# Optimization experiments

Hardware: AMD Instinct MI355X
Metric: run time of the kernel (lower is better)

Reference implementation:

```python
import jax, jax.numpy as jnp
import numpy as np

N = 4096
C = 8192
D = 64
MARGIN = 0.1
ALPHA = 32.0


def setup_inputs() -> dict:
    key = jax.random.key(0)
    k1, k2, k3, k4 = jax.random.split(key, 4)
    embeddings = jax.random.normal(k1, (N, D), dtype=jnp.float32)
    labels = jax.random.randint(k2, (N,), 0, C)
    # kaiming_normal_(mode='fan_out') on a (C, D) tensor -> std = sqrt(2/C)
    mean_proxies = jax.random.normal(k3, (C, D), dtype=jnp.float32) * np.sqrt(2.0 / C)
    log_variance_proxies = jax.random.normal(k4, (C, D), dtype=jnp.float32) * np.sqrt(2.0 / C)
    return {
        "embeddings": embeddings,
        "labels": labels,
        "mean_proxies": mean_proxies,
        "log_variance_proxies": log_variance_proxies,
    }


def _mls_scores(e, mu, logvar):
    """score[i,j] = -0.5 * sum_d[(e_id - mu_jd)^2 * exp(-logvar_jd) + logvar_jd].
    Expanded into GEMMs to avoid materializing the (N, C, D) broadcast tensor."""
    inv_var = jnp.exp(-logvar)                                  # (C, D)
    e2_term = (e * e) @ inv_var.T                               # (N, C)
    cross = e @ (mu * inv_var).T                                # (N, C)
    const = jnp.sum(mu * mu * inv_var + logvar, axis=1)         # (C,)
    return -0.5 * (e2_term - 2.0 * cross + const[None, :])      # (N, C)


def reference(embeddings, labels, mean_proxies, log_variance_proxies):
    score_mat = _mls_scores(embeddings, mean_proxies, log_variance_proxies)  # (N, C)
    pos_mask = jax.nn.one_hot(labels, C, dtype=score_mat.dtype)              # (N, C)

    pos_e = -ALPHA * (score_mat - MARGIN)
    neg_e = ALPHA * (score_mat + MARGIN)
    m = jnp.max(pos_e)  # NOTE: original code uses max(pos_exp) for BOTH terms
    pos_exp = jnp.exp(pos_e - m)
    neg_exp = jnp.exp(neg_e - m)

    counts = jnp.sum(pos_mask, axis=0)                   # (C,)
    num_valid = jnp.sum(counts != 0).astype(score_mat.dtype)

    pos_sim_sum = jnp.sum(jnp.where(pos_mask == 1, pos_exp, 0.0), axis=0)  # (C,)
    neg_sim_sum = jnp.sum(jnp.where(pos_mask == 0, neg_exp, 0.0), axis=0)  # (C,)

    pos_term = jnp.sum(jnp.log1p(pos_sim_sum) + m) / num_valid
    neg_term = jnp.sum(jnp.log1p(neg_sim_sum) + m) / C
    return pos_term + neg_term
```

## Files before the change

kernel.cpp:

```cpp
#include <hip/hip_runtime.h>
#include <hip/hip_bf16.h>
#include <math.h>


#define N_EMB 4096
#define C_CLS 8192
#define D_DIM 64
#define K_DIM 128

typedef __attribute__((ext_vector_type(8))) __bf16 bf16x8;
typedef __attribute__((ext_vector_type(4))) __bf16 bf16x4;
typedef __attribute__((ext_vector_type(16))) float f32x16;
typedef __attribute__((ext_vector_type(4))) int i32x4;

__device__ __forceinline__ void async_ld16(void* lds, const void* g) {
  __builtin_amdgcn_global_load_lds(
      (__attribute__((address_space(1))) void*)g,
      (__attribute__((address_space(3))) void*)lds, 16, 0, 0);
}

__global__ void k_prep(const float* __restrict__ emb,
                       const float* __restrict__ mp,
                       const float* __restrict__ lvp,
                       __bf16* __restrict__ wsA,
                       __bf16* __restrict__ wsB,
                       float* __restrict__ constv) {
  const int wave = (int)((blockIdx.x * blockDim.x + threadIdx.x) >> 6);
  const int lane = threadIdx.x & 63;
  const int sub = lane >> 4, q = lane & 15;
  const int row = wave * 4 + sub;
  if (row < N_EMB) {
    float4 e4 = *(const float4*)&emb[row * D_DIM + q * 4];
    bf16x4 sq = {(__bf16)(e4.x * e4.x), (__bf16)(e4.y * e4.y),
                 (__bf16)(e4.z * e4.z), (__bf16)(e4.w * e4.w)};
    bf16x4 ev = {(__bf16)e4.x, (__bf16)e4.y, (__bf16)e4.z, (__bf16)e4.w};
    *(bf16x4*)&wsA[row * K_DIM + q * 4] = sq;
    *(bf16x4*)&wsA[row * K_DIM + D_DIM + q * 4] = ev;
  } else {
    const int j = row - N_EMB;
    float4 mu4 = *(const float4*)&mp[j * D_DIM + q * 4];
    float4 lv4 = *(const float4*)&lvp[j * D_DIM + q * 4];
    float iv0 = __expf(-lv4.x), iv1 = __expf(-lv4.y);
    float iv2 = __expf(-lv4.z), iv3 = __expf(-lv4.w);
    bf16x4 ivv = {(__bf16)iv0, (__bf16)iv1, (__bf16)iv2, (__bf16)iv3};
    bf16x4 mv = {(__bf16)(-2.0f * mu4.x * iv0), (__bf16)(-2.0f * mu4.y * iv1),
                 (__bf16)(-2.0f * mu4.z * iv2), (__bf16)(-2.0f * mu4.w * iv3)};
    *(bf16x4*)&wsB[j * K_DIM + q * 4] = ivv;
    *(bf16x4*)&wsB[j * K_DIM + D_DIM + q * 4] = mv;
    float t = fmaf(mu4.x * mu4.x, iv0, lv4.x)
            + fmaf(mu4.y * mu4.y, iv1, lv4.y)
            + fmaf(mu4.z * mu4.z, iv2, lv4.z)
            + fmaf(mu4.w * mu4.w, iv3, lv4.w);
    #pragma unroll
    for (int s = 8; s >= 1; s >>= 1) t += __shfl_xor(t, s);
    if (q == 0) constv[j] = t;
  }
}

__global__ __launch_bounds__(256, 2) void k_main(
    const __bf16* __restrict__ wsA, const __bf16* __restrict__ wsB,
    const float* __restrict__ constv, const int* __restrict__ labels,
    float* __restrict__ wsM, float* __restrict__ wsP, float* __restrict__ wsN) {
  __shared__ __align__(16) char As[32768];
  __shared__ __align__(16) char Bs[32768];

  const int tid = threadIdx.x;
  const int rb = blockIdx.x & 31;
  const int cb = blockIdx.x >> 5;

  const char* Ag = (const char*)(wsA + (size_t)rb * 128 * K_DIM);
  const char* Bg = (const char*)(wsB + (size_t)cb * 128 * K_DIM);
  #pragma unroll
  for (int it = 0; it < 8; ++it) {
    int L = it * 256 + tid;
    int r = L >> 4, cs = L & 15;
    int goff = r * 256 + ((cs ^ (r & 15)) << 4);
    async_ld16(As + L * 16, Ag + goff);
  }
  #pragma unroll
  for (int it = 0; it < 8; ++it) {
    int L = it * 256 + tid;
    int r = L >> 4, cs = L & 15;
    int goff = r * 256 + ((cs ^ (r & 15)) << 4);
    async_ld16(Bs + L * 16, Bg + goff);
  }
  __syncthreads();

  const int wv = tid >> 6, lane = tid & 63;
  const int wr = wv >> 1, wc = wv & 1;
  const int l31 = lane & 31, kg = lane >> 5;
  const int l15 = lane & 15;

  f32x16 acc[2][2];
  #pragma unroll
  for (int mi = 0; mi < 2; ++mi)
    #pragma unroll
    for (int ni = 0; ni < 2; ++ni)
      #pragma unroll
      for (int r = 0; r < 16; ++r) acc[mi][ni][r] = 0.f;

  #pragma unroll
  for (int kk = 0; kk < 8; ++kk) {
    const int c = kk * 2 + kg;
    const int cofs = (c ^ l15) << 4;
    bf16x8 af[2], bfr[2];
    #pragma unroll
    for (int mi = 0; mi < 2; ++mi)
      af[mi] = *(const bf16x8*)(As + (wr * 64 + mi * 32 + l31) * 256 + cofs);
    #pragma unroll
    for (int ni = 0; ni < 2; ++ni)
      bfr[ni] = *(const bf16x8*)(Bs + (wc * 64 + ni * 32 + l31) * 256 + cofs);
    #pragma unroll
    for (int mi = 0; mi < 2; ++mi)
      #pragma unroll
      for (int ni = 0; ni < 2; ++ni)
        acc[mi][ni] = __builtin_amdgcn_mfma_f32_32x32x16_bf16(
            af[mi], bfr[ni], acc[mi][ni], 0, 0, 0);
  }

  __syncthreads();
  float* colred = (float*)As;
  int* labels_s = (int*)(As + 3072);
  float* pc_s   = (float*)(As + 3584);
  if (tid < 128) {
    labels_s[tid] = labels[rb * 128 + tid];
    pc_s[tid] = fmaf(16.0f, constv[cb * 128 + tid], 3.2f);
  }
  __syncthreads();

  i32x4 labv[2][4];
  #pragma unroll
  for (int mi = 0; mi < 2; ++mi)
    #pragma unroll
    for (int g = 0; g < 4; ++g)
      labv[mi][g] = *(const i32x4*)&labels_s[wr * 64 + mi * 32 + 4 * kg + 8 * g];

  #pragma unroll
  for (int ni = 0; ni < 2; ++ni) {
    const int col_local = wc * 64 + ni * 32 + l31;
    const int gcol = cb * 128 + col_local;
    const float pcv = pc_s[col_local];
    float lmax = -1e30f;
    #pragma unroll
    for (int mi = 0; mi < 2; ++mi)
      #pragma unroll
      for (int r = 0; r < 16; ++r)
        lmax = fmaxf(lmax, fmaf(16.0f, acc[mi][ni][r], pcv));
    lmax = fmaxf(lmax, __shfl_xor(lmax, 32));
    float ps = 0.f, ns = 0.f;
    #pragma unroll
    for (int mi = 0; mi < 2; ++mi)
      #pragma unroll
      for (int r = 0; r < 16; ++r) {
        float pe = fmaf(16.0f, acc[mi][ni][r], pcv);
        bool match = (labv[mi][r >> 2][r & 3] == gcol);
        float v = match ? pe : (6.4f - pe);
        float ex = __expf(v - lmax);
        ps += match ? ex : 0.f;
        ns += match ? 0.f : ex;
      }
    ps += __shfl_xor(ps, 32);
    ns += __shfl_xor(ns, 32);
    if (kg == 0) {
      float* cr = &colred[(wr * 128 + col_local) * 3];
      cr[0] = lmax; cr[1] = ps; cr[2] = ns;
    }
  }
  __syncthreads();
  if (tid < 128) {
    const float* c0 = &colred[(0 * 128 + tid) * 3];
    const float* c1 = &colred[(1 * 128 + tid) * 3];
    float M = fmaxf(c0[0], c1[0]);
    float s0 = __expf(c0[0] - M), s1 = __expf(c1[0] - M);
    int gcol = cb * 128 + tid;
    wsM[rb * C_CLS + gcol] = M;
    wsP[rb * C_CLS + gcol] = fmaf(c0[1], s0, c1[1] * s1);
    wsN[rb * C_CLS + gcol] = fmaf(c0[2], s0, c1[2] * s1);
  }
}

__global__ __launch_bounds__(256) void k_red1(
    const float* __restrict__ wsM, const float* __restrict__ wsP,
    const float* __restrict__ wsN, float* __restrict__ Mcol,
    float* __restrict__ Pcol, float* __restrict__ Ncol) {
  __shared__ float red[8][32][3];
  const int tid = threadIdx.x;
  const int col = tid & 31, part = tid >> 5;
  const int j = blockIdx.x * 32 + col;

  float m4[4];
  float M = -1e30f;
  #pragma unroll
  for (int r = 0; r < 4; ++r) {
    m4[r] = wsM[(part * 4 + r) * C_CLS + j];
    M = fmaxf(M, m4[r]);
  }
  float ps = 0.f, ns = 0.f;
  #pragma unroll
  for (int r = 0; r < 4; ++r) {
    float s = __expf(m4[r] - M);
    ps = fmaf(wsP[(part * 4 + r) * C_CLS + j], s, ps);
    ns = fmaf(wsN[(part * 4 + r) * C_CLS + j], s, ns);
  }
  red[part][col][0] = M; red[part][col][1] = ps; red[part][col][2] = ns;
  __syncthreads();
  if (part == 0) {
    float Mx = -1e30f;
    #pragma unroll
    for (int p = 0; p < 8; ++p) Mx = fmaxf(Mx, red[p][col][0]);
    float P = 0.f, Nn = 0.f;
    #pragma unroll
    for (int p = 0; p < 8; ++p) {
      float s = __expf(red[p][col][0] - Mx);
      P = fmaf(red[p][col][1], s, P);
      Nn = fmaf(red[p][col][2], s, Nn);
    }
    Mcol[j] = Mx; Pcol[j] = P; Ncol[j] = Nn;
  }
}

__global__ __launch_bounds__(1024) void k_fin(
    const float* __restrict__ Mcol, const float* __restrict__ Pcol,
    const float* __restrict__ Ncol, const int* __restrict__ labels,
    float* __restrict__ out) {
  __shared__ unsigned char flag[C_CLS];
  __shared__ float sA[16], sB[16];
  __shared__ int sI[16];
  const int tid = threadIdx.x;
  const int wv = tid >> 6, lane = tid & 63;

  float colMv[8], colPv[8], colNv[8];
  #pragma unroll
  for (int k = 0; k < 8; ++k) {
    int i = k * 1024 + tid;
    colMv[k] = Mcol[i]; colPv[k] = Pcol[i]; colNv[k] = Ncol[i];
  }

  for (int i = tid; i < C_CLS; i += 1024) flag[i] = 0;
  __syncthreads();
  for (int i = tid; i < N_EMB; i += 1024) flag[labels[i]] = 1;
  __syncthreads();
  int nv = 0;
  float gm = -1e30f;
  #pragma unroll
  for (int k = 0; k < 8; ++k) {
    nv += flag[k * 1024 + tid];
    gm = fmaxf(gm, colMv[k]);
  }
  #pragma unroll
  for (int s = 32; s >= 1; s >>= 1) {
    gm = fmaxf(gm, __shfl_xor(gm, s));
    nv += __shfl_xor(nv, s);
  }
  if (lane == 0) { sA[wv] = gm; sI[wv] = nv; }
  __syncthreads();
  if (tid == 0) {
    float mm = -1e30f; int n = 0;
    #pragma unroll
    for (int k = 0; k < 16; ++k) { mm = fmaxf(mm, sA[k]); n += sI[k]; }
    sA[0] = mm; sI[0] = n;
  }
  __syncthreads();
  const float m = sA[0];
  const int num_valid = sI[0];
  __syncthreads();
  float pt = 0.f, nt = 0.f;
  #pragma unroll
  for (int k = 0; k < 8; ++k) {
    float s = __expf(colMv[k] - m);
    pt += log1pf(colPv[k] * s);
    nt += log1pf(colNv[k] * s);
  }
  #pragma unroll
  for (int s = 32; s >= 1; s >>= 1) {
    pt += __shfl_xor(pt, s);
    nt += __shfl_xor(nt, s);
  }
  if (lane == 0) { sA[wv] = pt; sB[wv] = nt; }
  __syncthreads();
  if (tid == 0) {
    float sp = 0.f, sn = 0.f;
    #pragma unroll
    for (int k = 0; k < 16; ++k) { sp += sA[k]; sn += sB[k]; }
    out[0] = (sp + (float)C_CLS * m) / (float)num_valid
           + (sn + (float)C_CLS * m) / (float)C_CLS;
  }
}

extern "C" void kernel_launch(void* const* d_in, const int* in_sizes, int n_in,
                              void* d_out, int out_size, void* d_ws, size_t ws_size,
                              hipStream_t stream) {
  const float* emb    = (const float*)d_in[0];
  const int*   labels = (const int*)d_in[1];
  const float* mp     = (const float*)d_in[2];
  const float* lvp    = (const float*)d_in[3];
  float* out = (float*)d_out;

  char* ws = (char*)d_ws;
  __bf16* wsA   = (__bf16*)ws;
  __bf16* wsB   = (__bf16*)(ws + (1u << 20));
  float* constv = (float*)(ws + 3u * (1u << 20));
  float* wsM    = (float*)(ws + 3u * (1u << 20) + (1u << 15));
  float* wsP    = wsM + 32 * C_CLS;
  float* wsN    = wsP + 32 * C_CLS;
  float* Mcol   = wsN + 32 * C_CLS;
  float* Pcol   = Mcol + C_CLS;
  float* Ncol   = Pcol + C_CLS;

  hipLaunchKernelGGL(k_prep, dim3(768), dim3(256), 0, stream,
                     emb, mp, lvp, wsA, wsB, constv);
  hipLaunchKernelGGL(k_main, dim3((N_EMB / 128) * (C_CLS / 128)), dim3(256), 0, stream,
                     wsA, wsB, constv, labels, wsM, wsP, wsN);
  hipLaunchKernelGGL(k_red1, dim3(256), dim3(256), 0, stream,
                     wsM, wsP, wsN, Mcol, Pcol, Ncol);
  hipLaunchKernelGGL(k_fin, dim3(1), dim3(1024), 0, stream,
                     Mcol, Pcol, Ncol, labels, out);
}
```

Baseline: 101.7 us.

## Use base-2 exponent domain, prefetch labels early, distribute valid-class counting to reduction

Rescales the score computation into log2 units so the epilogue uses exp2f directly, storing the scaled scores back into the accumulators and folding the margin into a precomputed bias. Label and constant loads are issued before the barrier to overlap with the async tile loads. The valid-class flag computation moves from the single-block final kernel into the 256-block reduction kernel, which emits per-block counts, removing an 8K shared flag array and serial scatter from k_fin. This adds redundant label scans in each reduction block and changes the rounding behaviour slightly.

```diff
diff --git a/kernel.cpp b/kernel.cpp
--- a/kernel.cpp
+++ b/kernel.cpp
@@ -7,6 +7,11 @@
 #define C_CLS 8192
 #define D_DIM 64
 #define K_DIM 128
+
+#define S2_F    23.083120654223414f
+#define B2_F     4.616624130844683f
+#define NEGC2_F  9.233248261689366f
+#define LN2_F    0.6931471805599453f
 
 typedef __attribute__((ext_vector_type(8))) __bf16 bf16x8;
 typedef __attribute__((ext_vector_type(4))) __bf16 bf16x4;
@@ -84,6 +89,11 @@
     int goff = r * 256 + ((cs ^ (r & 15)) << 4);
     async_ld16(Bs + L * 16, Bg + goff);
   }
+  int lab_r = 0; float cv_r = 0.f;
+  if (tid < 128) {
+    lab_r = labels[rb * 128 + tid];
+    cv_r  = constv[cb * 128 + tid];
+  }
   __syncthreads();
 
   const int wv = tid >> 6, lane = tid & 63;
@@ -123,8 +133,8 @@
   int* labels_s = (int*)(As + 3072);
   float* pc_s   = (float*)(As + 3584);
   if (tid < 128) {
-    labels_s[tid] = labels[rb * 128 + tid];
-    pc_s[tid] = fmaf(16.0f, constv[cb * 128 + tid], 3.2f);
+    labels_s[tid] = lab_r;
+    pc_s[tid] = fmaf(S2_F, cv_r, B2_F);
   }
   __syncthreads();
 
@@ -144,18 +154,22 @@
     #pragma unroll
     for (int mi = 0; mi < 2; ++mi)
       #pragma unroll
-      for (int r = 0; r < 16; ++r)
-        lmax = fmaxf(lmax, fmaf(16.0f, acc[mi][ni][r], pcv));
+      for (int r = 0; r < 16; ++r) {
+        float pe = fmaf(S2_F, acc[mi][ni][r], pcv);
+        acc[mi][ni][r] = pe;
+        lmax = fmaxf(lmax, pe);
+      }
     lmax = fmaxf(lmax, __shfl_xor(lmax, 32));
+    const float negb = NEGC2_F - lmax;
     float ps = 0.f, ns = 0.f;
     #pragma unroll
     for (int mi = 0; mi < 2; ++mi)
       #pragma unroll
       for (int r = 0; r < 16; ++r) {
-        float pe = fmaf(16.0f, acc[mi][ni][r], pcv);
+        float pe = acc[mi][ni][r];
         bool match = (labv[mi][r >> 2][r & 3] == gcol);
-        float v = match ? pe : (6.4f - pe);
-        float ex = __expf(v - lmax);
+        float a = match ? (pe - lmax) : (negb - pe);
+        float ex = exp2f(a);
         ps += match ? ex : 0.f;
         ns += match ? 0.f : ex;
       }
@@ -171,7 +185,7 @@
     const float* c0 = &colred[(0 * 128 + tid) * 3];
     const float* c1 = &colred[(1 * 128 + tid) * 3];
     float M = fmaxf(c0[0], c1[0]);
-    float s0 = __expf(c0[0] - M), s1 = __expf(c1[0] - M);
+    float s0 = exp2f(c0[0] - M), s1 = exp2f(c1[0] - M);
     int gcol = cb * 128 + tid;
     wsM[rb * C_CLS + gcol] = M;
     wsP[rb * C_CLS + gcol] = fmaf(c0[1], s0, c1[1] * s1);
@@ -181,12 +195,17 @@
 
 __global__ __launch_bounds__(256) void k_red1(
     const float* __restrict__ wsM, const float* __restrict__ wsP,
-    const float* __restrict__ wsN, float* __restrict__ Mcol,
-    float* __restrict__ Pcol, float* __restrict__ Ncol) {
+    const float* __restrict__ wsN, const int* __restrict__ labels,
+    float* __restrict__ Mcol, float* __restrict__ Pcol,
+    float* __restrict__ Ncol, int* __restrict__ nvp) {
   __shared__ float red[8][32][3];
+  __shared__ int fl[32];
   const int tid = threadIdx.x;
   const int col = tid & 31, part = tid >> 5;
-  const int j = blockIdx.x * 32 + col;
+  const int bx = blockIdx.x;
+  const int j = bx * 32 + col;
+
+  if (tid < 32) fl[tid] = 0;
 
   float m4[4];
   float M = -1e30f;
@@ -198,12 +217,22 @@
   float ps = 0.f, ns = 0.f;
   #pragma unroll
   for (int r = 0; r < 4; ++r) {
-    float s = __expf(m4[r] - M);
+    float s = exp2f(m4[r] - M);
     ps = fmaf(wsP[(part * 4 + r) * C_CLS + j], s, ps);
     ns = fmaf(wsN[(part * 4 + r) * C_CLS + j], s, ns);
   }
   red[part][col][0] = M; red[part][col][1] = ps; red[part][col][2] = ns;
   __syncthreads();
+
+  #pragma unroll
+  for (int it = 0; it < 4; ++it) {
+    int4 lb = ((const int4*)labels)[it * 256 + tid];
+    if ((lb.x >> 5) == bx) fl[lb.x & 31] = 1;
+    if ((lb.y >> 5) == bx) fl[lb.y & 31] = 1;
+    if ((lb.z >> 5) == bx) fl[lb.z & 31] = 1;
+    if ((lb.w >> 5) == bx) fl[lb.w & 31] = 1;
+  }
+
   if (part == 0) {
     float Mx = -1e30f;
     #pragma unroll
@@ -211,19 +240,25 @@
     float P = 0.f, Nn = 0.f;
     #pragma unroll
     for (int p = 0; p < 8; ++p) {
-      float s = __expf(red[p][col][0] - Mx);
+      float s = exp2f(red[p][col][0] - Mx);
       P = fmaf(red[p][col][1], s, P);
       Nn = fmaf(red[p][col][2], s, Nn);
     }
     Mcol[j] = Mx; Pcol[j] = P; Ncol[j] = Nn;
   }
+  __syncthreads();
+  if (tid < 64) {
+    int f = (tid < 32) ? fl[tid] : 0;
+    #pragma unroll
+    for (int s = 32; s >= 1; s >>= 1) f += __shfl_xor(f, s);
+    if (tid == 0) nvp[bx] = f;
+  }
 }
 
 __global__ __launch_bounds__(1024) void k_fin(
     const float* __restrict__ Mcol, const float* __restrict__ Pcol,
-    const float* __restrict__ Ncol, const int* __restrict__ labels,
+    const float* __restrict__ Ncol, const int* __restrict__ nvp,
     float* __restrict__ out) {
-  __shared__ unsigned char flag[C_CLS];
   __shared__ float sA[16], sB[16];
   __shared__ int sI[16];
   const int tid = threadIdx.x;
@@ -235,18 +270,11 @@
     int i = k * 1024 + tid;
     colMv[k] = Mcol[i]; colPv[k] = Pcol[i]; colNv[k] = Ncol[i];
   }
-
-  for (int i = tid; i < C_CLS; i += 1024) flag[i] = 0;
-  __syncthreads();
-  for (int i = tid; i < N_EMB; i += 1024) flag[labels[i]] = 1;
-  __syncthreads();
-  int nv = 0;
+  int nv = (tid < 256) ? nvp[tid] : 0;
+
   float gm = -1e30f;
   #pragma unroll
-  for (int k = 0; k < 8; ++k) {
-    nv += flag[k * 1024 + tid];
-    gm = fmaxf(gm, colMv[k]);
-  }
+  for (int k = 0; k < 8; ++k) gm = fmaxf(gm, colMv[k]);
   #pragma unroll
   for (int s = 32; s >= 1; s >>= 1) {
     gm = fmaxf(gm, __shfl_xor(gm, s));
@@ -267,7 +295,7 @@
   float pt = 0.f, nt = 0.f;
   #pragma unroll
   for (int k = 0; k < 8; ++k) {
-    float s = __expf(colMv[k] - m);
+    float s = exp2f(colMv[k] - m);
     pt += log1pf(colPv[k] * s);
     nt += log1pf(colNv[k] * s);
   }
@@ -282,8 +310,9 @@
     float sp = 0.f, sn = 0.f;
     #pragma unroll
     for (int k = 0; k < 16; ++k) { sp += sA[k]; sn += sB[k]; }
-    out[0] = (sp + (float)C_CLS * m) / (float)num_valid
-           + (sn + (float)C_CLS * m) / (float)C_CLS;
+    const float mn = m * LN2_F;
+    out[0] = (sp + (float)C_CLS * mn) / (float)num_valid
+           + (sn + (float)C_CLS * mn) / (float)C_CLS;
   }
 }
 
@@ -306,13 +335,14 @@
   float* Mcol   = wsN + 32 * C_CLS;
   float* Pcol   = Mcol + C_CLS;
   float* Ncol   = Pcol + C_CLS;
+  int*   nvp    = (int*)(Ncol + C_CLS);
 
   hipLaunchKernelGGL(k_prep, dim3(768), dim3(256), 0, stream,
                      emb, mp, lvp, wsA, wsB, constv);
   hipLaunchKernelGGL(k_main, dim3((N_EMB / 128) * (C_CLS / 128)), dim3(256), 0, stream,
                      wsA, wsB, constv, labels, wsM, wsP, wsN);
   hipLaunchKernelGGL(k_red1, dim3(256), dim3(256), 0, stream,
-                     wsM, wsP, wsN, Mcol, Pcol, Ncol);
+                     wsM, wsP, wsN, labels, Mcol, Pcol, Ncol, nvp);
   hipLaunchKernelGGL(k_fin, dim3(1), dim3(1024), 0, stream,
-                     Mcol, Pcol, Ncol, labels, out);
-}
+                     Mcol, Pcol, Ncol, nvp, out);
+}
```

Result: slower. 104.5 us (+2.8%).
